# Performance work log

Hardware: AMD Instinct MI355X
Metric: run time of the kernel (lower is better)

## Reference

```python
import jax, jax.numpy as jnp
import numpy as np

B, L, H = 4, 4096, 1024
NH, W, SHIFT, FF = 16, 64, 32, 4096
HD = H // NH
EPS = 1e-5


def _ln(x, g, b):
    mu = jnp.mean(x, axis=-1, keepdims=True)
    var = jnp.var(x, axis=-1, keepdims=True)
    return (x - mu) * jax.lax.rsqrt(var + EPS) * g + b


def setup_inputs() -> dict:
    key = jax.random.key(0)
    ks = jax.random.split(key, 8)
    s = 0.02
    return {
        "x": jax.random.normal(ks[0], (B, L, H), dtype=jnp.float32),
        "ln1_g": jnp.ones((H,), jnp.float32),
        "ln1_b": jnp.zeros((H,), jnp.float32),
        "in_proj_w": jax.random.normal(ks[1], (3 * H, H), jnp.float32) * s,
        "in_proj_b": jnp.zeros((3 * H,), jnp.float32),
        "out_proj_w": jax.random.normal(ks[2], (H, H), jnp.float32) * s,
        "out_proj_b": jnp.zeros((H,), jnp.float32),
        "ln2_g": jnp.ones((H,), jnp.float32),
        "ln2_b": jnp.zeros((H,), jnp.float32),
        "w1": jax.random.normal(ks[3], (FF, H), jnp.float32) * s,
        "b1": jnp.zeros((FF,), jnp.float32),
        "w2": jax.random.normal(ks[4], (H, FF), jnp.float32) * s,
        "b2": jnp.zeros((H,), jnp.float32),
    }


def reference(x, ln1_g, ln1_b, in_proj_w, in_proj_b, out_proj_w, out_proj_b,
              ln2_g, ln2_b, w1, b1, w2, b2):
    # shift (torch.roll with negative shift)
    xs = jnp.roll(x, -SHIFT, axis=1)
    q_in = _ln(xs, ln1_g, ln1_b)
    # packed qkv projection (torch MHA in_proj)
    qkv = q_in @ in_proj_w.T + in_proj_b              # [B, L, 3H]
    q, k, v = jnp.split(qkv, 3, axis=-1)
    nW = L // W
    # block-diagonal mask == independent windows: [B, nW, W, NH, HD]
    def to_win(t):
        return t.reshape(B, nW, W, NH, HD)
    qw, kw, vw = to_win(q), to_win(k), to_win(v)
    scale = 1.0 / jnp.sqrt(jnp.float32(HD))
    scores = jnp.einsum('bnqhd,bnkhd->bnhqk', qw, kw) * scale
    attn = jax.nn.softmax(scores, axis=-1)
    o = jnp.einsum('bnhqk,bnkhd->bnqhd', attn, vw).reshape(B, L, H)
    o = o @ out_proj_w.T + out_proj_b
    xs = xs + o
    x = jnp.roll(xs, SHIFT, axis=1)  # un-shift
    z = _ln(x, ln2_g, ln2_b)
    z = jax.nn.gelu(z @ w1.T + b1, approximate=False) @ w2.T + b2
    return x + z
```

## Files before the change

kernel.cpp:

```cpp
#include <hip/hip_runtime.h>
#include <cstdint>
#include <cstddef>

#define B_ 4
#define L_ 4096
#define H_ 1024
#define NH_ 16
#define W_ 64
#define SHIFT_ 32
#define FF_ 4096
#define HD_ 64

typedef unsigned short u16;
typedef __attribute__((ext_vector_type(8))) __bf16 bf16x8;
typedef __attribute__((ext_vector_type(4))) float f32x4;
typedef __attribute__((ext_vector_type(4))) unsigned short u16x4;

__device__ __forceinline__ float bf2f(u16 u) {
    unsigned int x = ((unsigned int)u) << 16;
    float f;
    __builtin_memcpy(&f, &x, 4);
    return f;
}
__device__ __forceinline__ u16 f2bf(float f) {
    unsigned int u;
    __builtin_memcpy(&u, &f, 4);
    u = (u + 0x7fffu + ((u >> 16) & 1u)) >> 16;
    return (u16)u;
}

__device__ __forceinline__ void gload16(const u16* g, u16* l) {
    __builtin_amdgcn_global_load_lds(
        (const __attribute__((address_space(1))) void*)g,
        (__attribute__((address_space(3))) void*)l, 16, 0, 0);
}

__device__ __forceinline__ bf16x8 ldfrag(const u16* p) {
    uint4 v = *(const uint4*)p;
    bf16x8 r;
    __builtin_memcpy(&r, &v, 16);
    return r;
}

__device__ __forceinline__ f32x4 mfma16(bf16x8 a, bf16x8 b, f32x4 c) {
    return __builtin_amdgcn_mfma_f32_16x16x32_bf16(a, b, c, 0, 0, 0);
}

__global__ __launch_bounds__(256) void cvt_kernel(
    const float* __restrict__ src, u16* __restrict__ dst, int n4) {
    const int i = blockIdx.x * 256 + threadIdx.x;
    if (i < n4) {
        const float4 v = ((const float4*)src)[i];
        u16x4 o;
        o[0] = f2bf(v.x); o[1] = f2bf(v.y);
        o[2] = f2bf(v.z); o[3] = f2bf(v.w);
        ((u16x4*)dst)[i] = o;
    }
}

template <int GELU, int BIAS, int F32OUT>
__global__ __launch_bounds__(512, 2) void gemm256(
    const u16* __restrict__ A, const u16* __restrict__ Bm,
    int lda, int ldb, const float* __restrict__ bias,
    void* __restrict__ Cv, int N, int K) {
    __shared__ __align__(16) u16 sA0[16384];
    __shared__ __align__(16) u16 sA1[16384];
    __shared__ __align__(16) u16 sB0[16384];
    __shared__ __align__(16) u16 sB1[16384];

    const int tid = threadIdx.x;
    const int lane = tid & 63;
    const int wv = tid >> 6;
    const int wr = wv >> 2;
    const int wc = wv & 3;
    const int ln15 = lane & 15;
    const int quad = lane >> 4;
    const int mBase = blockIdx.y * 256;
    const int nBase = blockIdx.x * 256;
    const int nt = K >> 6;

    const int srow = tid >> 3;
    const int sk = ((tid & 7) ^ (srow & 7)) * 8;
    const u16* gA = A + (size_t)(mBase + srow) * lda + sk;
    const u16* gB = Bm + (size_t)(nBase + srow) * ldb + sk;
    const size_t ldas = (size_t)lda * 64;
    const size_t ldbs = (size_t)ldb * 64;

    const int rbA = (wr * 128 + ln15) * 64;
    const int rbB = (wc * 64 + ln15) * 64;
    const int sw0 = (quad ^ (ln15 & 7)) * 8;
    const int sw1 = ((4 + quad) ^ (ln15 & 7)) * 8;

    f32x4 acc[8][4] = {};

#define STAGE_T(g, ld64, buf)                          \
    do {                                               \
        const u16* _g = (g);                           \
        gload16(_g, (buf) + tid * 8);                  \
        gload16(_g + (ld64), (buf) + 4096 + tid * 8);  \
        gload16(_g + 2 * (ld64), (buf) + 8192 + tid * 8);  \
        gload16(_g + 3 * (ld64), (buf) + 12288 + tid * 8); \
    } while (0)

#define HALF(CA, CB, SW)                                             \
    do {                                                             \
        bf16x8 a_[8], b_[4];                                         \
        _Pragma("unroll") for (int fm = 0; fm < 8; ++fm)             \
            a_[fm] = ldfrag((CA) + rbA + fm * 1024 + (SW));          \
        _Pragma("unroll") for (int fn = 0; fn < 4; ++fn)             \
            b_[fn] = ldfrag((CB) + rbB + fn * 1024 + (SW));          \
        __builtin_amdgcn_s_setprio(1);                               \
        _Pragma("unroll") for (int fm = 0; fm < 8; ++fm)             \
            _Pragma("unroll") for (int fn = 0; fn < 4; ++fn)         \
                acc[fm][fn] = mfma16(a_[fm], b_[fn], acc[fm][fn]);   \
        __builtin_amdgcn_s_setprio(0);                               \
    } while (0)

#define TILE(CA, CB, PA, PB, tn)                            \
    do {                                                    \
        const bool _st = (tn) < nt;                         \
        if (_st) STAGE_T(gA + (size_t)(tn) * 64, ldas, PA); \
        HALF(CA, CB, sw0);                                  \
        if (_st) STAGE_T(gB + (size_t)(tn) * 64, ldbs, PB); \
        HALF(CA, CB, sw1);                                  \
        __syncthreads();                                    \
    } while (0)

    STAGE_T(gA, ldas, sA0);
    STAGE_T(gB, ldbs, sB0);
    __syncthreads();

    for (int t = 0; t < nt; t += 2) {
        TILE(sA0, sB0, sA1, sB1, t + 1);
        TILE(sA1, sB1, sA0, sB0, t + 2);
    }

    if (F32OUT) {
        float* C = (float*)Cv;
        const int r0 = mBase + wr * 128 + quad * 4;
        const int c0 = nBase + wc * 64 + ln15;
#pragma unroll
        for (int fn = 0; fn < 4; ++fn) {
            const int col = c0 + fn * 16;
            const float bcol = BIAS ? bias[col] : 0.0f;
#pragma unroll
            for (int fm = 0; fm < 8; ++fm) {
#pragma unroll
                for (int r = 0; r < 4; ++r) {
                    const int row = r0 + fm * 16 + r;
                    float v = acc[fm][fn][r] + bcol;
                    if (GELU) v = 0.5f * v * (1.0f + erff(v * 0.70710678118f));
                    C[(size_t)row * N + col] += v;
                }
            }
        }
    } else {
        u16* lo = wr ? sB0 : sA0;
        u16* hi = wr ? sB1 : sA1;
#pragma unroll
        for (int fn = 0; fn < 4; ++fn) {
            const int col = wc * 64 + fn * 16 + ln15;
            const float bcol = BIAS ? bias[nBase + col] : 0.0f;
#pragma unroll
            for (int fm = 0; fm < 8; ++fm) {
                u16* wb = (fm < 4) ? lo : hi;
#pragma unroll
                for (int r = 0; r < 4; ++r) {
                    float v = acc[fm][fn][r] + bcol;
                    if (GELU) v = 0.5f * v * (1.0f + erff(v * 0.70710678118f));
                    wb[((fm & 3) * 16 + quad * 4 + r) * 256 + col] = f2bf(v);
                }
            }
        }
        __syncthreads();
        u16* Cu = (u16*)Cv;
        const int rr = tid >> 5;
        const int cc = (tid & 31) * 8;
#pragma unroll
        for (int p = 0; p < 16; ++p) {
            const u16* rb = (p < 4) ? sA0 : (p < 8) ? sA1 : (p < 12) ? sB0 : sB1;
            const uint4 vv =
                *(const uint4*)(rb + ((p & 3) * 16 + rr) * 256 + cc);
            *(uint4*)(Cu + (size_t)(mBase + p * 16 + rr) * N + nBase + cc) = vv;
        }
    }
#undef TILE
#undef HALF
#undef STAGE_T
}

__global__ __launch_bounds__(256, 4) void ln1_kernel(
    const float* __restrict__ x, const float* __restrict__ g,
    const float* __restrict__ bb, u16* __restrict__ y) {
    const int row = blockIdx.x;
    const int bi = row >> 12, l = row & 4095;
    const float* src = x + ((size_t)(bi << 12) + ((l + SHIFT_) & 4095)) * 1024;
    const int t = threadIdx.x;
    const int lane = t & 63, wv = t >> 6;

    const float4 u = ((const float4*)src)[t];
    float v[4] = {u.x, u.y, u.z, u.w};
    float sum = 0.f, sq = 0.f;
#pragma unroll
    for (int k = 0; k < 4; ++k) { sum += v[k]; sq += v[k] * v[k]; }
    for (int off = 32; off > 0; off >>= 1) {
        sum += __shfl_down(sum, off);
        sq += __shfl_down(sq, off);
    }
    __shared__ float red[8];
    __shared__ float smu, srs;
    if (lane == 0) { red[wv] = sum; red[4 + wv] = sq; }
    __syncthreads();
    if (t == 0) {
        float s = red[0] + red[1] + red[2] + red[3];
        float q = red[4] + red[5] + red[6] + red[7];
        float mu = s * (1.0f / 1024.0f);
        float var = q * (1.0f / 1024.0f) - mu * mu;
        smu = mu;
        srs = rsqrtf(var + 1e-5f);
    }
    __syncthreads();
    const float mu = smu, rs = srs;
    const float4 gv = ((const float4*)g)[t];
    const float4 bv = ((const float4*)bb)[t];
    u16x4 outv;
    outv[0] = f2bf((v[0] - mu) * rs * gv.x + bv.x);
    outv[1] = f2bf((v[1] - mu) * rs * gv.y + bv.y);
    outv[2] = f2bf((v[2] - mu) * rs * gv.z + bv.z);
    outv[3] = f2bf((v[3] - mu) * rs * gv.w + bv.w);
    ((u16x4*)(y + (size_t)row * 1024))[t] = outv;
}

__global__ __launch_bounds__(256, 4) void ln2_kernel(
    const float* __restrict__ x, const u16* __restrict__ o2,
    const float* __restrict__ g, const float* __restrict__ bb,
    float* __restrict__ x2, u16* __restrict__ z) {
    const int row = blockIdx.x;
    const int bi = row >> 12, l = row & 4095;
    const size_t srcO = (size_t)(bi << 12) + ((l - SHIFT_) & 4095);
    const int t = threadIdx.x;
    const int lane = t & 63, wv = t >> 6;

    const float4 ux = ((const float4*)(x + (size_t)row * 1024))[t];
    const u16x4 uo = ((const u16x4*)(o2 + srcO * 1024))[t];
    float v[4];
    v[0] = ux.x + bf2f(uo[0]);
    v[1] = ux.y + bf2f(uo[1]);
    v[2] = ux.z + bf2f(uo[2]);
    v[3] = ux.w + bf2f(uo[3]);
    float sum = 0.f, sq = 0.f;
#pragma unroll
    for (int k = 0; k < 4; ++k) { sum += v[k]; sq += v[k] * v[k]; }
    float4 x2v = {v[0], v[1], v[2], v[3]};
    ((float4*)(x2 + (size_t)row * 1024))[t] = x2v;

    for (int off = 32; off > 0; off >>= 1) {
        sum += __shfl_down(sum, off);
        sq += __shfl_down(sq, off);
    }
    __shared__ float red[8];
    __shared__ float smu, srs;
    if (lane == 0) { red[wv] = sum; red[4 + wv] = sq; }
    __syncthreads();
    if (t == 0) {
        float s = red[0] + red[1] + red[2] + red[3];
        float q = red[4] + red[5] + red[6] + red[7];
        float mu = s * (1.0f / 1024.0f);
        float var = q * (1.0f / 1024.0f) - mu * mu;
        smu = mu;
        srs = rsqrtf(var + 1e-5f);
    }
    __syncthreads();
    const float mu = smu, rs = srs;
    const float4 gv = ((const float4*)g)[t];
    const float4 bv = ((const float4*)bb)[t];
    u16x4 outv;
    outv[0] = f2bf((v[0] - mu) * rs * gv.x + bv.x);
    outv[1] = f2bf((v[1] - mu) * rs * gv.y + bv.y);
    outv[2] = f2bf((v[2] - mu) * rs * gv.z + bv.z);
    outv[3] = f2bf((v[3] - mu) * rs * gv.w + bv.w);
    ((u16x4*)(z + (size_t)row * 1024))[t] = outv;
}

__global__ __launch_bounds__(256, 2) void attn_kernel(
    const u16* __restrict__ qkv, u16* __restrict__ o) {
    __shared__ __align__(16) u16 sQ[64 * 64];
    __shared__ __align__(16) u16 sK[64 * 64];
    __shared__ __align__(16) u16 sV[64 * 64];
    __shared__ float sS[64 * 66];

    const int t = threadIdx.x;
    const int win = blockIdx.x >> 4;
    const int head = blockIdx.x & 15;
    const size_t rowbase = (size_t)win * 64;
    const u16* base = qkv + rowbase * 3072 + head * 64;

    {
        const int c0 = t, c1 = t + 256;
        const int r0 = c0 >> 3, d0 = (c0 & 7) * 8;
        const int r1 = c1 >> 3, d1 = (c1 & 7) * 8;
        const u16* g0 = base + (size_t)r0 * 3072 + d0;
        const u16* g1 = base + (size_t)r1 * 3072 + d1;
        gload16(g0, &sQ[c0 * 8]);
        gload16(g1, &sQ[c1 * 8]);
        gload16(g0 + 1024, &sK[c0 * 8]);
        gload16(g1 + 1024, &sK[c1 * 8]);
        gload16(g0 + 2048, &sV[c0 * 8]);
        gload16(g1 + 2048, &sV[c1 * 8]);
    }
    __syncthreads();

    const int lane = t & 63, wv = t >> 6;
    const int ln15 = lane & 15, quad = lane >> 4;

    f32x4 accS[4] = {};
#pragma unroll
    for (int kb = 0; kb < 2; ++kb) {
        bf16x8 aF = ldfrag(&sQ[(wv * 16 + ln15) * 64 + kb * 32 + quad * 8]);
#pragma unroll
        for (int jt = 0; jt < 4; ++jt) {
            bf16x8 bF = ldfrag(&sK[(jt * 16 + ln15) * 64 + kb * 32 + quad * 8]);
            accS[jt] = mfma16(aF, bF, accS[jt]);
        }
    }
#pragma unroll
    for (int jt = 0; jt < 4; ++jt)
#pragma unroll
        for (int r = 0; r < 4; ++r)
            sS[(wv * 16 + quad * 4 + r) * 66 + jt * 16 + ln15] =
                accS[jt][r] * 0.125f;
    __syncthreads();

    {
        const int row = t >> 2, part = t & 3;
        const float* sr = &sS[row * 66 + part * 16];
        float vals[16];
        float mx = -1e30f;
#pragma unroll
        for (int i = 0; i < 16; ++i) {
            vals[i] = sr[i];
            mx = fmaxf(mx, vals[i]);
        }
        mx = fmaxf(mx, __shfl_xor(mx, 1));
        mx = fmaxf(mx, __shfl_xor(mx, 2));
        float sum = 0.f;
#pragma unroll
        for (int i = 0; i < 16; ++i) {
            vals[i] = __expf(vals[i] - mx);
            sum += vals[i];
        }
        sum += __shfl_xor(sum, 1);
        sum += __shfl_xor(sum, 2);
        const float inv = 1.0f / sum;
        u16* pr = &sQ[row * 64 + part * 16];
#pragma unroll
        for (int i = 0; i < 16; ++i) pr[i] = f2bf(vals[i] * inv);
    }
    __syncthreads();

    f32x4 accO[4] = {};
#pragma unroll
    for (int kb = 0; kb < 2; ++kb) {
        bf16x8 aF = ldfrag(&sQ[(wv * 16 + ln15) * 64 + kb * 32 + quad * 8]);
#pragma unroll
        for (int dt = 0; dt < 4; ++dt) {
            u16 tmp[8];
#pragma unroll
            for (int j = 0; j < 8; ++j)
                tmp[j] = sV[(kb * 32 + quad * 8 + j) * 64 + dt * 16 + ln15];
            bf16x8 bF;
            __builtin_memcpy(&bF, tmp, 16);
            accO[dt] = mfma16(aF, bF, accO[dt]);
        }
    }
    u16* ob = o + rowbase * 1024 + head * 64;
#pragma unroll
    for (int dt = 0; dt < 4; ++dt)
#pragma unroll
        for (int r = 0; r < 4; ++r) {
            const int q = wv * 16 + quad * 4 + r;
            const int d = dt * 16 + ln15;
            ob[(size_t)q * 1024 + d] = f2bf(accO[dt][r]);
        }
}

extern "C" void kernel_launch(void* const* d_in, const int* in_sizes, int n_in,
                              void* d_out, int out_size, void* d_ws,
                              size_t ws_size, hipStream_t stream) {
    (void)in_sizes; (void)n_in; (void)out_size; (void)ws_size;
    const float* x = (const float*)d_in[0];
    const float* ln1_g = (const float*)d_in[1];
    const float* ln1_b = (const float*)d_in[2];
    const float* in_proj_w = (const float*)d_in[3];
    const float* in_proj_b = (const float*)d_in[4];
    const float* out_proj_w = (const float*)d_in[5];
    const float* out_proj_b = (const float*)d_in[6];
    const float* ln2_g = (const float*)d_in[7];
    const float* ln2_b = (const float*)d_in[8];
    const float* w1 = (const float*)d_in[9];
    const float* b1 = (const float*)d_in[10];
    const float* w2 = (const float*)d_in[11];
    const float* b2 = (const float*)d_in[12];
    float* out = (float*)d_out;

    char* ws = (char*)d_ws;
    const size_t MB = 1024 * 1024;
    u16* wb_w1 = (u16*)(ws + 0 * MB);
    u16* wb_w2 = (u16*)(ws + 8 * MB);
    u16* wb_inproj = (u16*)(ws + 16 * MB);
    u16* wb_outproj = (u16*)(ws + 22 * MB);
    u16* qkv = (u16*)(ws + 24 * MB);
    u16* o2 = (u16*)(ws + 88 * MB);
    u16* z = (u16*)(ws + 16 * MB);
    u16* h_buf = (u16*)(ws + 48 * MB);

    u16* qin = (u16*)d_out;
    u16* o_full = (u16*)((char*)d_out + 32 * MB);
    float* x2 = out;

    const int M = B_ * L_;

    cvt_kernel<<<(FF_ * H_ / 4 + 255) / 256, 256, 0, stream>>>(
        w1, wb_w1, FF_ * H_ / 4);
    cvt_kernel<<<(H_ * FF_ / 4 + 255) / 256, 256, 0, stream>>>(
        w2, wb_w2, H_ * FF_ / 4);
    cvt_kernel<<<(3 * H_ * H_ / 4 + 255) / 256, 256, 0, stream>>>(
        in_proj_w, wb_inproj, 3 * H_ * H_ / 4);
    cvt_kernel<<<(H_ * H_ / 4 + 255) / 256, 256, 0, stream>>>(
        out_proj_w, wb_outproj, H_ * H_ / 4);

    ln1_kernel<<<M, 256, 0, stream>>>(x, ln1_g, ln1_b, qin);
    gemm256<0, 1, 0><<<dim3(3 * H_ / 256, M / 256), 512, 0, stream>>>(
        qin, wb_inproj, H_, H_, in_proj_b, qkv, 3 * H_, H_);
    attn_kernel<<<(M / W_) * NH_, 256, 0, stream>>>(qkv, o_full);
    gemm256<0, 1, 0><<<dim3(H_ / 256, M / 256), 512, 0, stream>>>(
        o_full, wb_outproj, H_, H_, out_proj_b, o2, H_, H_);

    ln2_kernel<<<M, 256, 0, stream>>>(x, o2, ln2_g, ln2_b, x2, z);

    gemm256<1, 1, 0><<<dim3(2048 / 256, M / 256), 512, 0, stream>>>(
        z, wb_w1, H_, H_, b1, h_buf, 2048, H_);
    gemm256<0, 0, 1><<<dim3(H_ / 256, M / 256), 512, 0, stream>>>(
        h_buf, wb_w2, 2048, FF_, nullptr, out, H_, 2048);
    gemm256<1, 1, 0><<<dim3(2048 / 256, M / 256), 512, 0, stream>>>(
        z, wb_w1 + (size_t)2048 * H_, H_, H_, b1 + 2048, h_buf, 2048, H_);
    gemm256<0, 1, 1><<<dim3(H_ / 256, M / 256), 512, 0, stream>>>(
        h_buf, wb_w2 + 2048, 2048, FF_, b2, out, H_, 2048);
}
```

Baseline: 851.0 us.

## Pipeline GEMM main loop into four phases with fine-grained waits and XCD swizzle

Rewrites the bf16 GEMM main loop so each K-tile runs in four sub-phases. Each phase interleaves LDS fragment loads, half-tile global prefetches of the next A/B tiles, explicit lgkmcnt/vmcnt waits and s_barriers. This replaces the older two halves with a full __syncthreads, aiming to hide global-load latency behind MFMA work. It also remaps workgroup IDs across groups of eight, presumably to match the MI355X's chiplet layout and improve L2 reuse. The cost is more barriers per tile and a fragile dependence on exact waitcnt counts and prefetch ordering.

```diff
diff --git a/kernel.cpp b/kernel.cpp
--- a/kernel.cpp
+++ b/kernel.cpp
@@ -75,16 +75,19 @@
     const int wc = wv & 3;
     const int ln15 = lane & 15;
     const int quad = lane >> 4;
-    const int mBase = blockIdx.y * 256;
-    const int nBase = blockIdx.x * 256;
+
+    const int gX = gridDim.x;
+    const int nwg = gX * gridDim.y;
+    int lin = blockIdx.y * gX + blockIdx.x;
+    if ((nwg & 7) == 0) lin = (lin & 7) * (nwg >> 3) + (lin >> 3);
+    const int mBase = (lin / gX) * 256;
+    const int nBase = (lin % gX) * 256;
     const int nt = K >> 6;
 
     const int srow = tid >> 3;
     const int sk = ((tid & 7) ^ (srow & 7)) * 8;
     const u16* gA = A + (size_t)(mBase + srow) * lda + sk;
     const u16* gB = Bm + (size_t)(nBase + srow) * ldb + sk;
-    const size_t ldas = (size_t)lda * 64;
-    const size_t ldbs = (size_t)ldb * 64;
 
     const int rbA = (wr * 128 + ln15) * 64;
     const int rbB = (wc * 64 + ln15) * 64;
@@ -93,46 +96,95 @@
 
     f32x4 acc[8][4] = {};
 
-#define STAGE_T(g, ld64, buf)                          \
-    do {                                               \
-        const u16* _g = (g);                           \
-        gload16(_g, (buf) + tid * 8);                  \
-        gload16(_g + (ld64), (buf) + 4096 + tid * 8);  \
-        gload16(_g + 2 * (ld64), (buf) + 8192 + tid * 8);  \
-        gload16(_g + 3 * (ld64), (buf) + 12288 + tid * 8); \
+#define STG(gp, ld, buf, h, t)                                          \
+    do {                                                                \
+        const u16* _g = (gp) + (size_t)((h)*128) * (ld) + (t) * 64;     \
+        u16* _d = (buf) + (h)*8192 + tid * 8;                           \
+        gload16(_g, _d);                                                \
+        gload16(_g + (size_t)64 * (ld), _d + 4096);                     \
     } while (0)
-
-#define HALF(CA, CB, SW)                                             \
-    do {                                                             \
-        bf16x8 a_[8], b_[4];                                         \
-        _Pragma("unroll") for (int fm = 0; fm < 8; ++fm)             \
-            a_[fm] = ldfrag((CA) + rbA + fm * 1024 + (SW));          \
-        _Pragma("unroll") for (int fn = 0; fn < 4; ++fn)             \
-            b_[fn] = ldfrag((CB) + rbB + fn * 1024 + (SW));          \
-        __builtin_amdgcn_s_setprio(1);                               \
-        _Pragma("unroll") for (int fm = 0; fm < 8; ++fm)             \
-            _Pragma("unroll") for (int fn = 0; fn < 4; ++fn)         \
-                acc[fm][fn] = mfma16(a_[fm], b_[fn], acc[fm][fn]);   \
-        __builtin_amdgcn_s_setprio(0);                               \
+#define LGK0                                            \
+    asm volatile("s_waitcnt lgkmcnt(0)" ::: "memory");  \
+    __builtin_amdgcn_sched_barrier(0)
+#define VMC4 asm volatile("s_waitcnt vmcnt(4)" ::: "memory")
+#define BAR __builtin_amdgcn_s_barrier()
+
+#define TILE_P(CA, CB, NB, tcur)                                        \
+    do {                                                                \
+        bf16x8 a0[8], a1[8], b0[4], b1[4];                              \
+                       \
+        _Pragma("unroll") for (int fm = 0; fm < 8; ++fm)                \
+            a0[fm] = ldfrag((CA) + rbA + fm * 1024 + sw0);              \
+        b0[0] = ldfrag((CB) + rbB + sw0);                               \
+        b0[1] = ldfrag((CB) + rbB + 1024 + sw0);                        \
+        if ((tcur) + 1 < nt) STG(gB, ldb, NB, 0, (tcur) + 1);           \
+        BAR;                                                            \
+        LGK0;                                                           \
+        __builtin_amdgcn_s_setprio(1);                                  \
+        _Pragma("unroll") for (int fm = 0; fm < 8; ++fm) {              \
+            acc[fm][0] = mfma16(a0[fm], b0[0], acc[fm][0]);             \
+            acc[fm][1] = mfma16(a0[fm], b0[1], acc[fm][1]);             \
+        }                                                               \
+        __builtin_amdgcn_s_setprio(0);                                  \
+        BAR;                                                            \
+                       \
+        b0[2] = ldfrag((CB) + rbB + 2048 + sw0);                        \
+        b0[3] = ldfrag((CB) + rbB + 3072 + sw0);                        \
+        _Pragma("unroll") for (int fm = 0; fm < 8; ++fm)                \
+            a1[fm] = ldfrag((CA) + rbA + fm * 1024 + sw1);              \
+        if ((tcur) + 1 < nt) STG(gB, ldb, NB, 1, (tcur) + 1);           \
+        BAR;                                                            \
+        LGK0;                                                           \
+        __builtin_amdgcn_s_setprio(1);                                  \
+        _Pragma("unroll") for (int fm = 0; fm < 8; ++fm) {              \
+            acc[fm][2] = mfma16(a0[fm], b0[2], acc[fm][2]);             \
+            acc[fm][3] = mfma16(a0[fm], b0[3], acc[fm][3]);             \
+        }                                                               \
+        __builtin_amdgcn_s_setprio(0);                                  \
+        BAR;                                                            \
+         \
+        b1[0] = ldfrag((CB) + rbB + sw1);                               \
+        b1[1] = ldfrag((CB) + rbB + 1024 + sw1);                        \
+        if ((tcur) + 2 < nt) STG(gA, lda, CA, 0, (tcur) + 2);           \
+        BAR;                                                            \
+        LGK0;                                                           \
+        __builtin_amdgcn_s_setprio(1);                                  \
+        _Pragma("unroll") for (int fm = 0; fm < 8; ++fm) {              \
+            acc[fm][0] = mfma16(a1[fm], b1[0], acc[fm][0]);             \
+            acc[fm][1] = mfma16(a1[fm], b1[1], acc[fm][1]);             \
+        }                                                               \
+        __builtin_amdgcn_s_setprio(0);                                  \
+        BAR;                                                            \
+                                  \
+        b1[2] = ldfrag((CB) + rbB + 2048 + sw1);                        \
+        b1[3] = ldfrag((CB) + rbB + 3072 + sw1);                        \
+        if ((tcur) + 2 < nt) STG(gA, lda, CA, 1, (tcur) + 2);           \
+        BAR;                                                            \
+        LGK0;                                                           \
+        __builtin_amdgcn_s_setprio(1);                                  \
+        _Pragma("unroll") for (int fm = 0; fm < 8; ++fm) {              \
+            acc[fm][2] = mfma16(a1[fm], b1[2], acc[fm][2]);             \
+            acc[fm][3] = mfma16(a1[fm], b1[3], acc[fm][3]);             \
+        }                                                               \
+        __builtin_amdgcn_s_setprio(0);                                  \
+        VMC4;                                                           \
+        BAR;                                                            \
     } while (0)
 
-#define TILE(CA, CB, PA, PB, tn)                            \
-    do {                                                    \
-        const bool _st = (tn) < nt;                         \
-        if (_st) STAGE_T(gA + (size_t)(tn) * 64, ldas, PA); \
-        HALF(CA, CB, sw0);                                  \
-        if (_st) STAGE_T(gB + (size_t)(tn) * 64, ldbs, PB); \
-        HALF(CA, CB, sw1);                                  \
-        __syncthreads();                                    \
-    } while (0)
-
-    STAGE_T(gA, ldas, sA0);
-    STAGE_T(gB, ldbs, sB0);
-    __syncthreads();
+    u16* mA = (u16*)sA0;
+    u16* mB = (u16*)sB0;
+    STG(gA, lda, mA, 0, 0);
+    STG(gA, lda, mA, 1, 0);
+    STG(gB, ldb, mB, 0, 0);
+    STG(gB, ldb, mB, 1, 0);
+    STG(gA, lda, sA1, 0, 1);
+    STG(gA, lda, sA1, 1, 1);
+    VMC4;
+    BAR;
 
     for (int t = 0; t < nt; t += 2) {
-        TILE(sA0, sB0, sA1, sB1, t + 1);
-        TILE(sA1, sB1, sA0, sB0, t + 2);
+        TILE_P(sA0, sB0, sB1, t);
+        TILE_P(sA1, sB1, sB0, t + 1);
     }
 
     if (F32OUT) {
@@ -179,14 +231,15 @@
 #pragma unroll
         for (int p = 0; p < 16; ++p) {
             const u16* rb = (p < 4) ? sA0 : (p < 8) ? sA1 : (p < 12) ? sB0 : sB1;
-            const uint4 vv =
-                *(const uint4*)(rb + ((p & 3) * 16 + rr) * 256 + cc);
+            const uint4 vv = *(const uint4*)(rb + ((p & 3) * 16 + rr) * 256 + cc);
             *(uint4*)(Cu + (size_t)(mBase + p * 16 + rr) * N + nBase + cc) = vv;
         }
     }
-#undef TILE
-#undef HALF
-#undef STAGE_T
+#undef TILE_P
+#undef BAR
+#undef VMC4
+#undef LGK0
+#undef STG
 }
 
 __global__ __launch_bounds__(256, 4) void ln1_kernel(
```

Measured after the change: 777.4 us. 1.09x faster.

## Switch GEMM to 32x32x16 MFMA with finer-grained pipelined staging and XCD-aware tile remap

Applied to the files above, without the earlier changes.

Rewrites the main 256x256 GEMM kernel to use 32x32x16 bf16 MFMA instead of 16x16x32. This cuts LDS fragment reads per FLOP. The staging schedule now uses explicit vmcnt/lgkmcnt waits and raw barriers, prefetching B for the next tile and A two tiles ahead, which spreads global-to-LDS traffic across the MFMA phases. Block indices are remapped so that consecutive workgroups are grouped by XCD, which is meant to improve L2 reuse. The hand-tuned waitcnt sequencing is risky: a miscounted vmcnt could cause a race.

```diff
diff --git a/kernel.cpp b/kernel.cpp
--- a/kernel.cpp
+++ b/kernel.cpp
@@ -14,6 +14,7 @@
 typedef unsigned short u16;
 typedef __attribute__((ext_vector_type(8))) __bf16 bf16x8;
 typedef __attribute__((ext_vector_type(4))) float f32x4;
+typedef __attribute__((ext_vector_type(16))) float f32x16;
 typedef __attribute__((ext_vector_type(4))) unsigned short u16x4;
 
 __device__ __forceinline__ float bf2f(u16 u) {
@@ -44,6 +45,9 @@
 
 __device__ __forceinline__ f32x4 mfma16(bf16x8 a, bf16x8 b, f32x4 c) {
     return __builtin_amdgcn_mfma_f32_16x16x32_bf16(a, b, c, 0, 0, 0);
+}
+__device__ __forceinline__ f32x16 mfma32(bf16x8 a, bf16x8 b, f32x16 c) {
+    return __builtin_amdgcn_mfma_f32_32x32x16_bf16(a, b, c, 0, 0, 0);
 }
 
 __global__ __launch_bounds__(256) void cvt_kernel(
@@ -73,81 +77,112 @@
     const int wv = tid >> 6;
     const int wr = wv >> 2;
     const int wc = wv & 3;
-    const int ln15 = lane & 15;
-    const int quad = lane >> 4;
-    const int mBase = blockIdx.y * 256;
-    const int nBase = blockIdx.x * 256;
+    const int ln31 = lane & 31;
+    const int hi = lane >> 5;
+
+    const int gX = gridDim.x;
+    const int nwg = gX * gridDim.y;
+    int lin = blockIdx.y * gX + blockIdx.x;
+    if ((nwg & 7) == 0) lin = (lin & 7) * (nwg >> 3) + (lin >> 3);
+    const int mBase = (lin / gX) * 256;
+    const int nBase = (lin % gX) * 256;
     const int nt = K >> 6;
 
     const int srow = tid >> 3;
     const int sk = ((tid & 7) ^ (srow & 7)) * 8;
     const u16* gA = A + (size_t)(mBase + srow) * lda + sk;
     const u16* gB = Bm + (size_t)(nBase + srow) * ldb + sk;
-    const size_t ldas = (size_t)lda * 64;
-    const size_t ldbs = (size_t)ldb * 64;
-
-    const int rbA = (wr * 128 + ln15) * 64;
-    const int rbB = (wc * 64 + ln15) * 64;
-    const int sw0 = (quad ^ (ln15 & 7)) * 8;
-    const int sw1 = ((4 + quad) ^ (ln15 & 7)) * 8;
-
-    f32x4 acc[8][4] = {};
-
-#define STAGE_T(g, ld64, buf)                          \
-    do {                                               \
-        const u16* _g = (g);                           \
-        gload16(_g, (buf) + tid * 8);                  \
-        gload16(_g + (ld64), (buf) + 4096 + tid * 8);  \
-        gload16(_g + 2 * (ld64), (buf) + 8192 + tid * 8);  \
-        gload16(_g + 3 * (ld64), (buf) + 12288 + tid * 8); \
+
+    const int rA = wr * 128 + ln31;
+    const int rB = wc * 64 + ln31;
+    const int swrA = rA & 7;
+    const int swrB = rB & 7;
+
+    f32x16 acc[4][2] = {};
+
+#define STG(gp, ld, buf, h, t)                                      \
+    do {                                                            \
+        const u16* _g = (gp) + (size_t)((h)*128) * (ld) + (t) * 64; \
+        u16* _d = (buf) + (h)*8192 + tid * 8;                       \
+        gload16(_g, _d);                                            \
+        gload16(_g + (size_t)64 * (ld), _d + 4096);                 \
     } while (0)
-
-#define HALF(CA, CB, SW)                                             \
-    do {                                                             \
-        bf16x8 a_[8], b_[4];                                         \
-        _Pragma("unroll") for (int fm = 0; fm < 8; ++fm)             \
-            a_[fm] = ldfrag((CA) + rbA + fm * 1024 + (SW));          \
-        _Pragma("unroll") for (int fn = 0; fn < 4; ++fn)             \
-            b_[fn] = ldfrag((CB) + rbB + fn * 1024 + (SW));          \
-        __builtin_amdgcn_s_setprio(1);                               \
-        _Pragma("unroll") for (int fm = 0; fm < 8; ++fm)             \
-            _Pragma("unroll") for (int fn = 0; fn < 4; ++fn)         \
-                acc[fm][fn] = mfma16(a_[fm], b_[fn], acc[fm][fn]);   \
-        __builtin_amdgcn_s_setprio(0);                               \
+#define LGK0                                           \
+    asm volatile("s_waitcnt lgkmcnt(0)" ::: "memory"); \
+    __builtin_amdgcn_sched_barrier(0)
+#define VMC4 asm volatile("s_waitcnt vmcnt(4)" ::: "memory")
+#define VMC0 asm volatile("s_waitcnt vmcnt(0)" ::: "memory")
+#define BAR __builtin_amdgcn_s_barrier()
+
+#define PHASE_READS(cA, cB, P)                                          \
+    _Pragma("unroll") for (int fm = 0; fm < 4; ++fm)                    \
+        _Pragma("unroll") for (int j = 0; j < 2; ++j)                   \
+            a_[fm][j] = ldfrag((cA) + (rA + fm * 32) * 64 +             \
+                               ((4 * (P) + 2 * j + hi) ^ swrA) * 8);    \
+    _Pragma("unroll") for (int fn = 0; fn < 2; ++fn)                    \
+        _Pragma("unroll") for (int j = 0; j < 2; ++j)                   \
+            b_[fn][j] = ldfrag((cB) + (rB + fn * 32) * 64 +             \
+                               ((4 * (P) + 2 * j + hi) ^ swrB) * 8)
+
+#define PHASE_MFMA                                                      \
+    __builtin_amdgcn_s_setprio(1);                                      \
+    _Pragma("unroll") for (int j = 0; j < 2; ++j)                       \
+        _Pragma("unroll") for (int fm = 0; fm < 4; ++fm)                \
+            _Pragma("unroll") for (int fn = 0; fn < 2; ++fn)            \
+                acc[fm][fn] = mfma32(a_[fm][j], b_[fn][j], acc[fm][fn]); \
+    __builtin_amdgcn_s_setprio(0)
+
+#define TILE32(cA, cB, oB, t)                        \
+    do {                                             \
+        bf16x8 a_[4][2], b_[2][2];                   \
+        PHASE_READS(cA, cB, 0);                      \
+        if ((t) + 1 < nt) {                          \
+            STG(gB, ldb, oB, 0, (t) + 1);            \
+            STG(gB, ldb, oB, 1, (t) + 1);            \
+        }                                            \
+        BAR;                                         \
+        LGK0;                                        \
+        PHASE_MFMA;                                  \
+        PHASE_READS(cA, cB, 1);                      \
+        BAR;                                         \
+        LGK0;                                        \
+        PHASE_MFMA;                                  \
+        if ((t) + 2 < nt) {                          \
+            STG(gA, lda, cA, 0, (t) + 2);            \
+            STG(gA, lda, cA, 1, (t) + 2);            \
+            VMC4;                                    \
+        } else {                                     \
+            VMC0;                                    \
+        }                                            \
+        BAR;                                         \
     } while (0)
 
-#define TILE(CA, CB, PA, PB, tn)                            \
-    do {                                                    \
-        const bool _st = (tn) < nt;                         \
-        if (_st) STAGE_T(gA + (size_t)(tn) * 64, ldas, PA); \
-        HALF(CA, CB, sw0);                                  \
-        if (_st) STAGE_T(gB + (size_t)(tn) * 64, ldbs, PB); \
-        HALF(CA, CB, sw1);                                  \
-        __syncthreads();                                    \
-    } while (0)
-
-    STAGE_T(gA, ldas, sA0);
-    STAGE_T(gB, ldbs, sB0);
-    __syncthreads();
+    STG(gA, lda, sA0, 0, 0);
+    STG(gA, lda, sA0, 1, 0);
+    STG(gB, ldb, sB0, 0, 0);
+    STG(gB, ldb, sB0, 1, 0);
+    STG(gA, lda, sA1, 0, 1);
+    STG(gA, lda, sA1, 1, 1);
+    VMC4;
+    BAR;
 
     for (int t = 0; t < nt; t += 2) {
-        TILE(sA0, sB0, sA1, sB1, t + 1);
-        TILE(sA1, sB1, sA0, sB0, t + 2);
+        TILE32(sA0, sB0, sB1, t);
+        TILE32(sA1, sB1, sB0, t + 1);
     }
 
     if (F32OUT) {
         float* C = (float*)Cv;
-        const int r0 = mBase + wr * 128 + quad * 4;
-        const int c0 = nBase + wc * 64 + ln15;
-#pragma unroll
-        for (int fn = 0; fn < 4; ++fn) {
-            const int col = c0 + fn * 16;
-            const float bcol = BIAS ? bias[col] : 0.0f;
-#pragma unroll
-            for (int fm = 0; fm < 8; ++fm) {
-#pragma unroll
-                for (int r = 0; r < 4; ++r) {
-                    const int row = r0 + fm * 16 + r;
+#pragma unroll
+        for (int fm = 0; fm < 4; ++fm) {
+#pragma unroll
+            for (int fn = 0; fn < 2; ++fn) {
+                const int col = nBase + wc * 64 + fn * 32 + ln31;
+                const float bcol = BIAS ? bias[col] : 0.0f;
+#pragma unroll
+                for (int r = 0; r < 16; ++r) {
+                    const int row = mBase + wr * 128 + fm * 32 + (r & 3) +
+                                    8 * (r >> 2) + 4 * hi;
                     float v = acc[fm][fn][r] + bcol;
                     if (GELU) v = 0.5f * v * (1.0f + erff(v * 0.70710678118f));
                     C[(size_t)row * N + col] += v;
@@ -155,20 +190,21 @@
             }
         }
     } else {
-        u16* lo = wr ? sB0 : sA0;
-        u16* hi = wr ? sB1 : sA1;
-#pragma unroll
-        for (int fn = 0; fn < 4; ++fn) {
-            const int col = wc * 64 + fn * 16 + ln15;
-            const float bcol = BIAS ? bias[nBase + col] : 0.0f;
-#pragma unroll
-            for (int fm = 0; fm < 8; ++fm) {
-                u16* wb = (fm < 4) ? lo : hi;
-#pragma unroll
-                for (int r = 0; r < 4; ++r) {
+        u16* e0 = wr ? sB0 : sA0;
+        u16* e1 = wr ? sB1 : sA1;
+#pragma unroll
+        for (int fm = 0; fm < 4; ++fm) {
+            u16* eb = (fm < 2) ? e0 : e1;
+#pragma unroll
+            for (int fn = 0; fn < 2; ++fn) {
+                const int C2 = wc * 64 + fn * 32 + ln31;
+                const float bcol = BIAS ? bias[nBase + C2] : 0.0f;
+#pragma unroll
+                for (int r = 0; r < 16; ++r) {
+                    const int rloc = (r & 3) + 8 * (r >> 2) + 4 * hi;
                     float v = acc[fm][fn][r] + bcol;
                     if (GELU) v = 0.5f * v * (1.0f + erff(v * 0.70710678118f));
-                    wb[((fm & 3) * 16 + quad * 4 + r) * 256 + col] = f2bf(v);
+                    eb[((fm & 1) * 32 + rloc) * 256 + C2] = f2bf(v);
                 }
             }
         }
@@ -179,14 +215,18 @@
 #pragma unroll
         for (int p = 0; p < 16; ++p) {
             const u16* rb = (p < 4) ? sA0 : (p < 8) ? sA1 : (p < 12) ? sB0 : sB1;
-            const uint4 vv =
-                *(const uint4*)(rb + ((p & 3) * 16 + rr) * 256 + cc);
+            const uint4 vv = *(const uint4*)(rb + ((p & 3) * 16 + rr) * 256 + cc);
             *(uint4*)(Cu + (size_t)(mBase + p * 16 + rr) * N + nBase + cc) = vv;
         }
     }
-#undef TILE
-#undef HALF
-#undef STAGE_T
+#undef TILE32
+#undef PHASE_MFMA
+#undef PHASE_READS
+#undef BAR
+#undef VMC0
+#undef VMC4
+#undef LGK0
+#undef STG
 }
 
 __global__ __launch_bounds__(256, 4) void ln1_kernel(
```

Result: faster. 804.1 us (-5.5%).

## Restructure GEMM main loop with explicit waitcnt pipelining and XCD-aware block remap

Applied to the files above, without the earlier changes.

Reworks the 256x256 bf16 GEMM mainloop so the global-to-LDS loads for A and B are issued at staggered points, with hand-placed vmcnt/lgkmcnt waits and raw s_barrier in place of __syncthreads. The aim is to keep loads for the next tiles in flight while MFMAs run. It also remaps the linear block index across groups of eight so neighbouring tiles land on the same XCD, which should improve L2 reuse. In exchange it adds more barriers per tile and relies on fragile manual wait counts that must stay correct for the async load counts.

```diff
diff --git a/kernel.cpp b/kernel.cpp
--- a/kernel.cpp
+++ b/kernel.cpp
@@ -75,16 +75,19 @@
     const int wc = wv & 3;
     const int ln15 = lane & 15;
     const int quad = lane >> 4;
-    const int mBase = blockIdx.y * 256;
-    const int nBase = blockIdx.x * 256;
+
+    const int gX = gridDim.x;
+    const int nwg = gX * gridDim.y;
+    int lin = blockIdx.y * gX + blockIdx.x;
+    if ((nwg & 7) == 0) lin = (lin & 7) * (nwg >> 3) + (lin >> 3);
+    const int mBase = (lin / gX) * 256;
+    const int nBase = (lin % gX) * 256;
     const int nt = K >> 6;
 
     const int srow = tid >> 3;
     const int sk = ((tid & 7) ^ (srow & 7)) * 8;
     const u16* gA = A + (size_t)(mBase + srow) * lda + sk;
     const u16* gB = Bm + (size_t)(nBase + srow) * ldb + sk;
-    const size_t ldas = (size_t)lda * 64;
-    const size_t ldbs = (size_t)ldb * 64;
 
     const int rbA = (wr * 128 + ln15) * 64;
     const int rbB = (wc * 64 + ln15) * 64;
@@ -93,46 +96,74 @@
 
     f32x4 acc[8][4] = {};
 
-#define STAGE_T(g, ld64, buf)                          \
-    do {                                               \
-        const u16* _g = (g);                           \
-        gload16(_g, (buf) + tid * 8);                  \
-        gload16(_g + (ld64), (buf) + 4096 + tid * 8);  \
-        gload16(_g + 2 * (ld64), (buf) + 8192 + tid * 8);  \
-        gload16(_g + 3 * (ld64), (buf) + 12288 + tid * 8); \
+#define STG(gp, ld, buf, h, t)                                      \
+    do {                                                            \
+        const u16* _g = (gp) + (size_t)((h)*128) * (ld) + (t) * 64; \
+        u16* _d = (buf) + (h)*8192 + tid * 8;                       \
+        gload16(_g, _d);                                            \
+        gload16(_g + (size_t)64 * (ld), _d + 4096);                 \
     } while (0)
-
-#define HALF(CA, CB, SW)                                             \
-    do {                                                             \
-        bf16x8 a_[8], b_[4];                                         \
-        _Pragma("unroll") for (int fm = 0; fm < 8; ++fm)             \
-            a_[fm] = ldfrag((CA) + rbA + fm * 1024 + (SW));          \
-        _Pragma("unroll") for (int fn = 0; fn < 4; ++fn)             \
-            b_[fn] = ldfrag((CB) + rbB + fn * 1024 + (SW));          \
-        __builtin_amdgcn_s_setprio(1);                               \
-        _Pragma("unroll") for (int fm = 0; fm < 8; ++fm)             \
-            _Pragma("unroll") for (int fn = 0; fn < 4; ++fn)         \
-                acc[fm][fn] = mfma16(a_[fm], b_[fn], acc[fm][fn]);   \
-        __builtin_amdgcn_s_setprio(0);                               \
+#define LGK0                                           \
+    asm volatile("s_waitcnt lgkmcnt(0)" ::: "memory"); \
+    __builtin_amdgcn_sched_barrier(0)
+#define VMC4 asm volatile("s_waitcnt vmcnt(4)" ::: "memory")
+#define VMC0 asm volatile("s_waitcnt vmcnt(0)" ::: "memory")
+#define BAR __builtin_amdgcn_s_barrier()
+
+#define TILE2(CA, CB, OB, t)                                        \
+    do {                                                            \
+        bf16x8 a0[8], a1[8], b0[4], b1[4];                          \
+           \
+        _Pragma("unroll") for (int fm = 0; fm < 8; ++fm)            \
+            a0[fm] = ldfrag((CA) + rbA + fm * 1024 + sw0);          \
+        _Pragma("unroll") for (int fn = 0; fn < 4; ++fn)            \
+            b0[fn] = ldfrag((CB) + rbB + fn * 1024 + sw0);          \
+        if ((t) + 1 < nt) {                                         \
+            STG(gB, ldb, OB, 0, (t) + 1);                           \
+            STG(gB, ldb, OB, 1, (t) + 1);                           \
+        }                                                           \
+        BAR;                                                        \
+        LGK0;                                                       \
+        __builtin_amdgcn_s_setprio(1);                              \
+        _Pragma("unroll") for (int fm = 0; fm < 8; ++fm)            \
+            _Pragma("unroll") for (int fn = 0; fn < 4; ++fn)        \
+                acc[fm][fn] = mfma16(a0[fm], b0[fn], acc[fm][fn]);  \
+        __builtin_amdgcn_s_setprio(0);                              \
+             \
+        _Pragma("unroll") for (int fm = 0; fm < 8; ++fm)            \
+            a1[fm] = ldfrag((CA) + rbA + fm * 1024 + sw1);          \
+        _Pragma("unroll") for (int fn = 0; fn < 4; ++fn)            \
+            b1[fn] = ldfrag((CB) + rbB + fn * 1024 + sw1);          \
+        BAR;                                                        \
+        LGK0;                                                       \
+        __builtin_amdgcn_s_setprio(1);                              \
+        _Pragma("unroll") for (int fm = 0; fm < 8; ++fm)            \
+            _Pragma("unroll") for (int fn = 0; fn < 4; ++fn)        \
+                acc[fm][fn] = mfma16(a1[fm], b1[fn], acc[fm][fn]);  \
+        __builtin_amdgcn_s_setprio(0);                              \
+        BAR;  \
+        if ((t) + 2 < nt) {                                         \
+            STG(gA, lda, CA, 0, (t) + 2);                           \
+            STG(gA, lda, CA, 1, (t) + 2);                           \
+            VMC4;                                                   \
+        } else {                                                    \
+            VMC0;                                                   \
+        }                                                           \
+        BAR;                                                        \
     } while (0)
 
-#define TILE(CA, CB, PA, PB, tn)                            \
-    do {                                                    \
-        const bool _st = (tn) < nt;                         \
-        if (_st) STAGE_T(gA + (size_t)(tn) * 64, ldas, PA); \
-        HALF(CA, CB, sw0);                                  \
-        if (_st) STAGE_T(gB + (size_t)(tn) * 64, ldbs, PB); \
-        HALF(CA, CB, sw1);                                  \
-        __syncthreads();                                    \
-    } while (0)
-
-    STAGE_T(gA, ldas, sA0);
-    STAGE_T(gB, ldbs, sB0);
-    __syncthreads();
+    STG(gA, lda, sA0, 0, 0);
+    STG(gA, lda, sA0, 1, 0);
+    STG(gB, ldb, sB0, 0, 0);
+    STG(gB, ldb, sB0, 1, 0);
+    STG(gA, lda, sA1, 0, 1);
+    STG(gA, lda, sA1, 1, 1);
+    VMC4;
+    BAR;
 
     for (int t = 0; t < nt; t += 2) {
-        TILE(sA0, sB0, sA1, sB1, t + 1);
-        TILE(sA1, sB1, sA0, sB0, t + 2);
+        TILE2(sA0, sB0, sB1, t);
+        TILE2(sA1, sB1, sB0, t + 1);
     }
 
     if (F32OUT) {
@@ -179,14 +210,16 @@
 #pragma unroll
         for (int p = 0; p < 16; ++p) {
             const u16* rb = (p < 4) ? sA0 : (p < 8) ? sA1 : (p < 12) ? sB0 : sB1;
-            const uint4 vv =
-                *(const uint4*)(rb + ((p & 3) * 16 + rr) * 256 + cc);
+            const uint4 vv = *(const uint4*)(rb + ((p & 3) * 16 + rr) * 256 + cc);
             *(uint4*)(Cu + (size_t)(mBase + p * 16 + rr) * N + nBase + cc) = vv;
         }
     }
-#undef TILE
-#undef HALF
-#undef STAGE_T
+#undef TILE2
+#undef BAR
+#undef VMC0
+#undef VMC4
+#undef LGK0
+#undef STG
 }
 
 __global__ __launch_bounds__(256, 4) void ln1_kernel(
```

Result: no change. 864.1 us (+1.5%).
